# Kernel tuning notes

Hardware: AMD Instinct MI355X
Metric: run time of the kernel (lower is better)

The kernel has to match this reference:

```python
import jax, jax.numpy as jnp
import numpy as np

TEMPERATURE = 0.5  # init temperature; attn_drop=0.0 so dropout is identity


def setup_inputs() -> dict:
    key = jax.random.key(0)
    k1, k2, k3 = jax.random.split(key, 3)
    B, H, N, D = 4, 8, 2048, 64
    q = jax.random.normal(k1, (B, H, N, D), dtype=jnp.float32)
    k = jax.random.normal(k2, (B, H, N, D), dtype=jnp.float32)
    v = jax.random.normal(k3, (B, H, N, D), dtype=jnp.float32)
    scale = jnp.asarray(D ** -0.5, dtype=jnp.float32)
    return {"q": q, "k": k, "v": v, "scale": scale}


def reference(q, k, v, scale):
    # logits: [B,H,N,N]
    logits = jnp.einsum("bhqd,bhkd->bhqk", q, k) * scale
    # first softmax acts as a soft mask over keys
    soft_mask = jax.nn.softmax(logits / TEMPERATURE, axis=-1)
    # second softmax over masked logits (elementwise product, NOT matmul)
    attn = jax.nn.softmax(logits * soft_mask, axis=-1)
    # dropout with p=0.0 is identity
    out = jnp.einsum("bhqk,bhkd->bhqd", attn, v)
    return out
```

## Files before the change

### kernel.cpp

```cpp
#include <hip/hip_runtime.h>


typedef _Float16 f16;
typedef f16 f16x8 __attribute__((ext_vector_type(8)));
typedef float f32x16 __attribute__((ext_vector_type(16)));

#define MFMA32(a, b, c) __builtin_amdgcn_mfma_f32_32x32x16_f16((a), (b), (c), 0, 0, 0)
#define EXP2(x) __builtin_amdgcn_exp2f(x)

#define N_CTX 2048
#define DH 64
#define KT 64
#define NKT (N_CTX / KT)
#define ROWS 256
#define QS 72
#define HEAD_ELEMS (N_CTX * DH)
#define C2 2.885390081777927f

__device__ inline unsigned pk(float a, float b) {
    typedef __fp16 fp16x2_t __attribute__((ext_vector_type(2)));
    union { fp16x2_t v; unsigned u; } x;
    x.v = __builtin_amdgcn_cvt_pkrtz(a, b);
    return x.u;
}

__device__ inline void load16_lds(const f16* g, f16* l) {
    __builtin_amdgcn_global_load_lds(
        (const __attribute__((address_space(1))) void*)g,
        (__attribute__((address_space(3))) void*)l, 16, 0, 0);
}

__global__ __launch_bounds__(256)
void cvt_kv(const float* __restrict__ k, const float* __restrict__ v,
            f16* __restrict__ ko, f16* __restrict__ vto) {
    __shared__ float Vs[64][65];
    const int bh = blockIdx.x & 31;
    const int kt = blockIdx.x >> 5;
    const int t  = threadIdx.x;
    const float* kb = k + (size_t)bh * HEAD_ELEMS + (size_t)kt * KT * DH;
    f16* kob = ko + (size_t)bh * HEAD_ELEMS + (size_t)kt * KT * DH;
    #pragma unroll
    for (int it = 0; it < 2; ++it) {
        int i = (it * 256 + t) * 8;
        float4 a = *(const float4*)&kb[i];
        float4 b = *(const float4*)&kb[i + 4];
        *(uint4*)&kob[i] = make_uint4(pk(a.x, a.y), pk(a.z, a.w), pk(b.x, b.y), pk(b.z, b.w));
    }
    const float* vb = v + (size_t)bh * HEAD_ELEMS + (size_t)kt * KT * DH;
    #pragma unroll
    for (int it = 0; it < 4; ++it) {
        int idx = it * 256 + t;
        int row = idx >> 4, c4 = idx & 15;
        *(float4*)&Vs[row][c4 * 4] = *(const float4*)&vb[row * DH + c4 * 4];
    }
    __syncthreads();
    int d = t >> 2, sub = t & 3;
    unsigned w[8];
    #pragma unroll
    for (int j = 0; j < 8; ++j) {
        int c = sub * 8 + j;
        w[j] = pk(Vs[c][d], Vs[c + 32][d]);
    }
    f16* ob = vto + (size_t)bh * HEAD_ELEMS + (size_t)d * N_CTX + kt * KT + sub * 16;
    *(uint4*)(ob)     = make_uint4(w[0], w[1], w[2], w[3]);
    *(uint4*)(ob + 8) = make_uint4(w[4], w[5], w[6], w[7]);
}

__global__ __launch_bounds__(512, 4)
void stk_attn_mfma(const float* __restrict__ qg, const f16* __restrict__ kh,
                   const f16* __restrict__ vth, const float* __restrict__ sg,
                   float* __restrict__ og) {
    __shared__ f16 QsPs[ROWS * QS];
    __shared__ f16 Ks[2][KT * DH];
    __shared__ f16 Vt[2][DH * KT];

    const int tid  = threadIdx.x;
    const int wv   = tid >> 6;
    const int lane = tid & 63;
    const int l31  = lane & 31;
    const int lh   = lane >> 5;
    const int bh   = blockIdx.x & 31;
    const int q0   = (blockIdx.x >> 5) * ROWS;
    const float scale2 = sg[0] * C2;

    const float* qb = qg + (size_t)bh * HEAD_ELEMS;
    const f16*   kb = kh + (size_t)bh * HEAD_ELEMS;
    const f16*   vtb = vth + (size_t)bh * HEAD_ELEMS;
    float*       ob = og + (size_t)bh * HEAD_ELEMS;

    #pragma unroll
    for (int it = 0; it < 8; ++it) {
        int idx = it * 512 + tid;
        int row = idx >> 4, c4 = idx & 15;
        float4 v = *(const float4*)&qb[((size_t)(q0 + row)) * DH + c4 * 4];
        *(uint2*)&QsPs[row * QS + c4 * 4] =
            make_uint2(pk(v.x * scale2, v.y * scale2), pk(v.z * scale2, v.w * scale2));
    }
    __syncthreads();

    f16x8 aq[4];
    #pragma unroll
    for (int km = 0; km < 4; ++km)
        aq[km] = *(const f16x8*)&QsPs[(wv * 32 + l31) * QS + km * 16 + lh * 8];

    const int c0   = wv * 64 + lane;
    const int key0 = c0 >> 3;
    const int swz  = ((c0 & 7) ^ (key0 & 7)) * 8;
    const int ks_src0 = key0 * DH + swz;
    const long vt_src0 = (long)key0 * N_CTX + swz;
    const int dst0 = wv * 512;
    const int x8 = l31 & 7;
    int xo[4];
    #pragma unroll
    for (int km = 0; km < 4; ++km) xo[km] = ((2 * km + lh) ^ x8) * 8;
    const int gb0 = l31 * 64, gb1 = (32 + l31) * 64;
    f16* const ps_wv = &QsPs[wv * 32 * QS];

    float s1[16] = {0};
    load16_lds(kb + ks_src0, &Ks[0][dst0]);
    __syncthreads();
    for (int kt = 0; kt < NKT; ++kt) {
        const int cur = kt & 1;
        if (kt + 1 < NKT)
            load16_lds(kb + (kt + 1) * (KT * DH) + ks_src0, &Ks[cur ^ 1][dst0]);
        #pragma unroll
        for (int kg = 0; kg < 2; ++kg) {
            const int gb = kg ? gb1 : gb0;
            f32x16 acc;
            #pragma unroll
            for (int i = 0; i < 16; ++i) acc[i] = 0.f;
            #pragma unroll
            for (int km = 0; km < 4; ++km) {
                f16x8 b = *(const f16x8*)&Ks[cur][gb + xo[km]];
                acc = MFMA32(aq[km], b, acc);
            }
            #pragma unroll
            for (int r = 0; r < 16; ++r)
                s1[r] += EXP2(acc[r]);
        }
        __syncthreads();
    }
    float inv1[16];
    #pragma unroll
    for (int r = 0; r < 16; ++r) {
        float v = s1[r];
        v += __shfl_xor(v, 1, 64);
        v += __shfl_xor(v, 2, 64);
        v += __shfl_xor(v, 4, 64);
        v += __shfl_xor(v, 8, 64);
        v += __shfl_xor(v, 16, 64);
        inv1[r] = 0.5f / v;
    }

    float l2[16] = {0};
    f32x16 O0, O1;
    #pragma unroll
    for (int i = 0; i < 16; ++i) { O0[i] = 0.f; O1[i] = 0.f; }

    load16_lds(kb + ks_src0, &Ks[0][dst0]);
    load16_lds(vtb + vt_src0, &Vt[0][dst0]);
    __syncthreads();
    for (int kt = 0; kt < NKT; ++kt) {
        const int cur = kt & 1;
        if (kt + 1 < NKT) {
            load16_lds(kb + (kt + 1) * (KT * DH) + ks_src0, &Ks[cur ^ 1][dst0]);
            load16_lds(vtb + vt_src0 + (kt + 1) * KT, &Vt[cur ^ 1][dst0]);
        }
        f32x16 a0, a1;
        #pragma unroll
        for (int i = 0; i < 16; ++i) { a0[i] = 0.f; a1[i] = 0.f; }
        #pragma unroll
        for (int km = 0; km < 4; ++km) {
            f16x8 b0 = *(const f16x8*)&Ks[cur][gb0 + xo[km]];
            f16x8 b1 = *(const f16x8*)&Ks[cur][gb1 + xo[km]];
            a0 = MFMA32(aq[km], b0, a0);
            a1 = MFMA32(aq[km], b1, a1);
        }
        #pragma unroll
        for (int r = 0; r < 16; ++r) {
            int row_r = (r & 3) + 8 * (r >> 2) + 4 * lh;
            float e10 = EXP2(a0[r]);
            float e20 = EXP2((a0[r] * e10) * inv1[r]);
            float e11 = EXP2(a1[r]);
            float e21 = EXP2((a1[r] * e11) * inv1[r]);
            l2[r] += e20 + e21;
            *(unsigned*)&ps_wv[row_r * QS + 2 * l31] = pk(e20, e21);
        }
        #pragma unroll
        for (int km = 0; km < 4; ++km) {
            f16x8 ap = *(const f16x8*)&ps_wv[l31 * QS + km * 16 + lh * 8];
            f16x8 bv0 = *(const f16x8*)&Vt[cur][gb0 + xo[km]];
            f16x8 bv1 = *(const f16x8*)&Vt[cur][gb1 + xo[km]];
            O0 = MFMA32(ap, bv0, O0);
            O1 = MFMA32(ap, bv1, O1);
        }
        __syncthreads();
    }

    float invl2[16];
    #pragma unroll
    for (int r = 0; r < 16; ++r) {
        float v = l2[r];
        v += __shfl_xor(v, 1, 64);
        v += __shfl_xor(v, 2, 64);
        v += __shfl_xor(v, 4, 64);
        v += __shfl_xor(v, 8, 64);
        v += __shfl_xor(v, 16, 64);
        invl2[r] = 1.0f / v;
    }
    #pragma unroll
    for (int r = 0; r < 16; ++r) {
        int row = q0 + wv * 32 + (r & 3) + 8 * (r >> 2) + 4 * lh;
        ob[(size_t)row * DH + l31]      = O0[r] * invl2[r];
        ob[(size_t)row * DH + 32 + l31] = O1[r] * invl2[r];
    }
}

extern "C" void kernel_launch(void* const* d_in, const int* in_sizes, int n_in,
                              void* d_out, int out_size, void* d_ws, size_t ws_size,
                              hipStream_t stream) {
    const float* q = (const float*)d_in[0];
    const float* k = (const float*)d_in[1];
    const float* v = (const float*)d_in[2];
    const float* s = (const float*)d_in[3];
    float* out = (float*)d_out;
    f16* kf  = (f16*)d_ws;
    f16* vtf = (f16*)((char*)d_ws + 8388608);
    cvt_kv<<<1024, 256, 0, stream>>>(k, v, kf, vtf);
    dim3 grid(32 * 8);
    stk_attn_mfma<<<grid, 512, 0, stream>>>(q, kf, vtf, s, out);
}
```

Before: 200.9 us.

## Split key tiles across wave pairs and halve rows per block to double grid

Each block now handles 128 query rows instead of 256, and the grid doubles to 512 blocks. Every pair of waves shares a 32-row group and splits the 64-key tile in half. Row sums and partial outputs are combined across the pair through shared memory reductions. The V transpose layout changes to interleave adjacent keys so the half-tile P·V MFMA reads line up. The aim is to fill more of the GPU's compute units and give each wave less work, at the cost of extra LDS traffic, extra barriers and twice as many K/V reloads across blocks.

```diff
diff --git a/kernel.cpp b/kernel.cpp
--- a/kernel.cpp
+++ b/kernel.cpp
@@ -12,8 +12,9 @@
 #define DH 64
 #define KT 64
 #define NKT (N_CTX / KT)
-#define ROWS 256
+#define ROWS 128
 #define QS 72
+#define PSS 40
 #define HEAD_ELEMS (N_CTX * DH)
 #define C2 2.885390081777927f
 
@@ -57,10 +58,8 @@
     int d = t >> 2, sub = t & 3;
     unsigned w[8];
     #pragma unroll
-    for (int j = 0; j < 8; ++j) {
-        int c = sub * 8 + j;
-        w[j] = pk(Vs[c][d], Vs[c + 32][d]);
-    }
+    for (int j = 0; j < 8; ++j)
+        w[j] = pk(Vs[sub * 16 + 2 * j][d], Vs[sub * 16 + 2 * j + 1][d]);
     f16* ob = vto + (size_t)bh * HEAD_ELEMS + (size_t)d * N_CTX + kt * KT + sub * 16;
     *(uint4*)(ob)     = make_uint4(w[0], w[1], w[2], w[3]);
     *(uint4*)(ob + 8) = make_uint4(w[4], w[5], w[6], w[7]);
@@ -70,30 +69,36 @@
 void stk_attn_mfma(const float* __restrict__ qg, const f16* __restrict__ kh,
                    const f16* __restrict__ vth, const float* __restrict__ sg,
                    float* __restrict__ og) {
-    __shared__ f16 QsPs[ROWS * QS];
-    __shared__ f16 Ks[2][KT * DH];
-    __shared__ f16 Vt[2][DH * KT];
+    __shared__ __align__(16) unsigned char smem[72704];
+    f16* const Qs   = (f16*)(smem);
+    f16* const KsB  = (f16*)(smem + 18432);
+    f16* const VtB  = (f16*)(smem + 34816);
+    f16* const PsB  = (f16*)(smem + 51200);
+    float* const sred = (float*)(smem + 71680);
+    float* const Ored = (float*)(smem + 18432);
 
     const int tid  = threadIdx.x;
     const int wv   = tid >> 6;
     const int lane = tid & 63;
     const int l31  = lane & 31;
     const int lh   = lane >> 5;
+    const int rg   = wv >> 1;
+    const int h    = wv & 1;
     const int bh   = blockIdx.x & 31;
     const int q0   = (blockIdx.x >> 5) * ROWS;
     const float scale2 = sg[0] * C2;
 
-    const float* qb = qg + (size_t)bh * HEAD_ELEMS;
-    const f16*   kb = kh + (size_t)bh * HEAD_ELEMS;
+    const float* qb  = qg + (size_t)bh * HEAD_ELEMS;
+    const f16*   kb  = kh + (size_t)bh * HEAD_ELEMS;
     const f16*   vtb = vth + (size_t)bh * HEAD_ELEMS;
-    float*       ob = og + (size_t)bh * HEAD_ELEMS;
-
-    #pragma unroll
-    for (int it = 0; it < 8; ++it) {
+    float*       ob  = og + (size_t)bh * HEAD_ELEMS;
+
+    #pragma unroll
+    for (int it = 0; it < 4; ++it) {
         int idx = it * 512 + tid;
         int row = idx >> 4, c4 = idx & 15;
         float4 v = *(const float4*)&qb[((size_t)(q0 + row)) * DH + c4 * 4];
-        *(uint2*)&QsPs[row * QS + c4 * 4] =
+        *(uint2*)&Qs[row * QS + c4 * 4] =
             make_uint2(pk(v.x * scale2, v.y * scale2), pk(v.z * scale2, v.w * scale2));
     }
     __syncthreads();
@@ -101,7 +106,7 @@
     f16x8 aq[4];
     #pragma unroll
     for (int km = 0; km < 4; ++km)
-        aq[km] = *(const f16x8*)&QsPs[(wv * 32 + l31) * QS + km * 16 + lh * 8];
+        aq[km] = *(const f16x8*)&Qs[(rg * 32 + l31) * QS + km * 16 + lh * 8];
 
     const int c0   = wv * 64 + lane;
     const int key0 = c0 >> 3;
@@ -109,38 +114,39 @@
     const int ks_src0 = key0 * DH + swz;
     const long vt_src0 = (long)key0 * N_CTX + swz;
     const int dst0 = wv * 512;
+    const int kbase = (h * 32 + l31) * 64;
     const int x8 = l31 & 7;
     int xo[4];
     #pragma unroll
     for (int km = 0; km < 4; ++km) xo[km] = ((2 * km + lh) ^ x8) * 8;
-    const int gb0 = l31 * 64, gb1 = (32 + l31) * 64;
-    f16* const ps_wv = &QsPs[wv * 32 * QS];
+    int vxo[2][2];
+    #pragma unroll
+    for (int g = 0; g < 2; ++g)
+        #pragma unroll
+        for (int km = 0; km < 2; ++km)
+            vxo[g][km] = (g * 32 + l31) * 64 + (((h * 4 + km * 2 + lh) ^ x8) * 8);
+    f16* const ps_wv = PsB + wv * (32 * PSS);
 
     float s1[16] = {0};
-    load16_lds(kb + ks_src0, &Ks[0][dst0]);
+    load16_lds(kb + ks_src0, KsB + dst0);
     __syncthreads();
     for (int kt = 0; kt < NKT; ++kt) {
-        const int cur = kt & 1;
+        const int cur = (kt & 1) * 4096;
         if (kt + 1 < NKT)
-            load16_lds(kb + (kt + 1) * (KT * DH) + ks_src0, &Ks[cur ^ 1][dst0]);
-        #pragma unroll
-        for (int kg = 0; kg < 2; ++kg) {
-            const int gb = kg ? gb1 : gb0;
-            f32x16 acc;
-            #pragma unroll
-            for (int i = 0; i < 16; ++i) acc[i] = 0.f;
-            #pragma unroll
-            for (int km = 0; km < 4; ++km) {
-                f16x8 b = *(const f16x8*)&Ks[cur][gb + xo[km]];
-                acc = MFMA32(aq[km], b, acc);
-            }
-            #pragma unroll
-            for (int r = 0; r < 16; ++r)
-                s1[r] += EXP2(acc[r]);
-        }
+            load16_lds(kb + (kt + 1) * (KT * DH) + ks_src0, KsB + (4096 - cur) + dst0);
+        f32x16 acc;
+        #pragma unroll
+        for (int i = 0; i < 16; ++i) acc[i] = 0.f;
+        #pragma unroll
+        for (int km = 0; km < 4; ++km) {
+            f16x8 b = *(const f16x8*)&KsB[cur + kbase + xo[km]];
+            acc = MFMA32(aq[km], b, acc);
+        }
+        #pragma unroll
+        for (int r = 0; r < 16; ++r)
+            s1[r] += EXP2(acc[r]);
         __syncthreads();
     }
-    float inv1[16];
     #pragma unroll
     for (int r = 0; r < 16; ++r) {
         float v = s1[r];
@@ -149,55 +155,65 @@
         v += __shfl_xor(v, 4, 64);
         v += __shfl_xor(v, 8, 64);
         v += __shfl_xor(v, 16, 64);
-        inv1[r] = 0.5f / v;
-    }
+        s1[r] = v;
+    }
+    if (l31 == 0) {
+        #pragma unroll
+        for (int r = 0; r < 16; ++r)
+            sred[(rg * 2 + h) * 32 + (r & 3) + 8 * (r >> 2) + 4 * lh] = s1[r];
+    }
+    __syncthreads();
+    float inv1[16];
+    #pragma unroll
+    for (int r = 0; r < 16; ++r) {
+        int row_r = (r & 3) + 8 * (r >> 2) + 4 * lh;
+        float tot = sred[(rg * 2) * 32 + row_r] + sred[(rg * 2 + 1) * 32 + row_r];
+        inv1[r] = 0.5f / tot;
+    }
+    __syncthreads();
 
     float l2[16] = {0};
     f32x16 O0, O1;
     #pragma unroll
     for (int i = 0; i < 16; ++i) { O0[i] = 0.f; O1[i] = 0.f; }
 
-    load16_lds(kb + ks_src0, &Ks[0][dst0]);
-    load16_lds(vtb + vt_src0, &Vt[0][dst0]);
+    load16_lds(kb + ks_src0, KsB + dst0);
+    load16_lds(vtb + vt_src0, VtB + dst0);
     __syncthreads();
     for (int kt = 0; kt < NKT; ++kt) {
-        const int cur = kt & 1;
+        const int cur = (kt & 1) * 4096;
         if (kt + 1 < NKT) {
-            load16_lds(kb + (kt + 1) * (KT * DH) + ks_src0, &Ks[cur ^ 1][dst0]);
-            load16_lds(vtb + vt_src0 + (kt + 1) * KT, &Vt[cur ^ 1][dst0]);
-        }
-        f32x16 a0, a1;
-        #pragma unroll
-        for (int i = 0; i < 16; ++i) { a0[i] = 0.f; a1[i] = 0.f; }
+            load16_lds(kb + (kt + 1) * (KT * DH) + ks_src0, KsB + (4096 - cur) + dst0);
+            load16_lds(vtb + vt_src0 + (kt + 1) * KT, VtB + (4096 - cur) + dst0);
+        }
+        f32x16 acc;
+        #pragma unroll
+        for (int i = 0; i < 16; ++i) acc[i] = 0.f;
         #pragma unroll
         for (int km = 0; km < 4; ++km) {
-            f16x8 b0 = *(const f16x8*)&Ks[cur][gb0 + xo[km]];
-            f16x8 b1 = *(const f16x8*)&Ks[cur][gb1 + xo[km]];
-            a0 = MFMA32(aq[km], b0, a0);
-            a1 = MFMA32(aq[km], b1, a1);
+            f16x8 b = *(const f16x8*)&KsB[cur + kbase + xo[km]];
+            acc = MFMA32(aq[km], b, acc);
         }
         #pragma unroll
         for (int r = 0; r < 16; ++r) {
+            float a  = acc[r];
+            float e1 = EXP2(a);
+            float e2 = EXP2((a * e1) * inv1[r]);
+            l2[r] += e2;
             int row_r = (r & 3) + 8 * (r >> 2) + 4 * lh;
-            float e10 = EXP2(a0[r]);
-            float e20 = EXP2((a0[r] * e10) * inv1[r]);
-            float e11 = EXP2(a1[r]);
-            float e21 = EXP2((a1[r] * e11) * inv1[r]);
-            l2[r] += e20 + e21;
-            *(unsigned*)&ps_wv[row_r * QS + 2 * l31] = pk(e20, e21);
-        }
-        #pragma unroll
-        for (int km = 0; km < 4; ++km) {
-            f16x8 ap = *(const f16x8*)&ps_wv[l31 * QS + km * 16 + lh * 8];
-            f16x8 bv0 = *(const f16x8*)&Vt[cur][gb0 + xo[km]];
-            f16x8 bv1 = *(const f16x8*)&Vt[cur][gb1 + xo[km]];
+            ps_wv[row_r * PSS + l31] = (f16)e2;
+        }
+        #pragma unroll
+        for (int km = 0; km < 2; ++km) {
+            f16x8 ap = *(const f16x8*)&ps_wv[l31 * PSS + km * 16 + lh * 8];
+            f16x8 bv0 = *(const f16x8*)&VtB[cur + vxo[0][km]];
+            f16x8 bv1 = *(const f16x8*)&VtB[cur + vxo[1][km]];
             O0 = MFMA32(ap, bv0, O0);
             O1 = MFMA32(ap, bv1, O1);
         }
         __syncthreads();
     }
 
-    float invl2[16];
     #pragma unroll
     for (int r = 0; r < 16; ++r) {
         float v = l2[r];
@@ -206,13 +222,42 @@
         v += __shfl_xor(v, 4, 64);
         v += __shfl_xor(v, 8, 64);
         v += __shfl_xor(v, 16, 64);
-        invl2[r] = 1.0f / v;
-    }
-    #pragma unroll
-    for (int r = 0; r < 16; ++r) {
-        int row = q0 + wv * 32 + (r & 3) + 8 * (r >> 2) + 4 * lh;
-        ob[(size_t)row * DH + l31]      = O0[r] * invl2[r];
-        ob[(size_t)row * DH + 32 + l31] = O1[r] * invl2[r];
+        l2[r] = v;
+    }
+    if (l31 == 0) {
+        #pragma unroll
+        for (int r = 0; r < 16; ++r)
+            sred[(rg * 2 + h) * 32 + (r & 3) + 8 * (r >> 2) + 4 * lh] = l2[r];
+    }
+    __syncthreads();
+    float invl2[16];
+    #pragma unroll
+    for (int r = 0; r < 16; ++r) {
+        int row_r = (r & 3) + 8 * (r >> 2) + 4 * lh;
+        float tot = sred[(rg * 2) * 32 + row_r] + sred[(rg * 2 + 1) * 32 + row_r];
+        invl2[r] = 1.0f / tot;
+    }
+
+    __syncthreads();
+    if (h == 1) {
+        #pragma unroll
+        for (int r = 0; r < 16; ++r) {
+            int row_r = (r & 3) + 8 * (r >> 2) + 4 * lh;
+            Ored[(rg * 32 + row_r) * 64 + l31]      = O0[r];
+            Ored[(rg * 32 + row_r) * 64 + 32 + l31] = O1[r];
+        }
+    }
+    __syncthreads();
+    if (h == 0) {
+        #pragma unroll
+        for (int r = 0; r < 16; ++r) {
+            int row_r = (r & 3) + 8 * (r >> 2) + 4 * lh;
+            int row = q0 + rg * 32 + row_r;
+            float o0 = O0[r] + Ored[(rg * 32 + row_r) * 64 + l31];
+            float o1 = O1[r] + Ored[(rg * 32 + row_r) * 64 + 32 + l31];
+            ob[(size_t)row * DH + l31]      = o0 * invl2[r];
+            ob[(size_t)row * DH + 32 + l31] = o1 * invl2[r];
+        }
     }
 }
 
@@ -227,6 +272,6 @@
     f16* kf  = (f16*)d_ws;
     f16* vtf = (f16*)((char*)d_ws + 8388608);
     cvt_kv<<<1024, 256, 0, stream>>>(k, v, kf, vtf);
-    dim3 grid(32 * 8);
+    dim3 grid(32 * 16);
     stk_attn_mfma<<<grid, 512, 0, stream>>>(q, kf, vtf, s, out);
 }
```

Result: faster. 179.3 us (-10.7%).
